# Kernel optimization log

Measured on AMD Instinct MI355X. Metric: run time of the kernel, lower is better.

Reference implementation:

```python
import jax, jax.numpy as jnp
import numpy as np

B, S, D, H, KD, FF = 512, 128, 128, 8, 128, 512  # molecules, max atoms, embed, heads, key_dim(=embed), ffn
NEG = -1e9
EPS = 1e-3  # keras LayerNormalization default epsilon


def _layernorm(x, g, b):
    m = jnp.mean(x, axis=-1, keepdims=True)
    v = jnp.var(x, axis=-1, keepdims=True)
    return (x - m) * jax.lax.rsqrt(v + EPS) * g + b


def setup_inputs() -> dict:
    key = jax.random.key(0)
    k = jax.random.split(key, 8)
    # ragged molecule sizes in [32, 128]; deterministic so shapes are reproducible
    counts = 32 + ((np.arange(B) * 37) % 97)
    N = int(counts.sum())  # 40914
    mol = jnp.asarray(np.repeat(np.arange(B), counts), jnp.int32)  # sorted molecule ids
    picked = jnp.asarray((np.arange(B) * 13) % counts, jnp.int64)  # valid in-molecule atom index
    s = 0.05
    return {
        "atom_features": jax.random.normal(k[0], (N, D), jnp.float32),
        "Wq": jax.random.normal(k[1], (D, H, KD), jnp.float32) * s,
        "bq": jnp.zeros((H, KD), jnp.float32),
        "Wk": jax.random.normal(k[2], (D, H, KD), jnp.float32) * s,
        "bk": jnp.zeros((H, KD), jnp.float32),
        "Wv": jax.random.normal(k[3], (D, H, KD), jnp.float32) * s,
        "bv": jnp.zeros((H, KD), jnp.float32),
        "Wo": jax.random.normal(k[4], (H, KD, D), jnp.float32) * s,
        "bo": jnp.zeros((D,), jnp.float32),
        "W1": jax.random.normal(k[5], (D, FF), jnp.float32) * s,
        "b1": jnp.zeros((FF,), jnp.float32),
        "W2": jax.random.normal(k[6], (FF, D), jnp.float32) * s,
        "b2": jnp.zeros((D,), jnp.float32),
        "g1": jnp.ones((D,), jnp.float32),
        "beta1": jnp.zeros((D,), jnp.float32),
        "g2": jnp.ones((D,), jnp.float32),
        "beta2": jnp.zeros((D,), jnp.float32),
        "molecule_indicator": mol,
        "picked_atoms": picked,
    }


def _forward(atom_features, Wq, bq, Wk, bk, Wv, bv, Wo, bo, W1, b1, W2, b2,
             g1, beta1, g2, beta2, mol, picked):
    N = mol.shape[0]
    # --- PartitionPadding: pack ragged atoms -> [B, S, D] (every molecule nonempty,
    # so the zero-row filter keeps all B molecules in order) ---
    counts = jax.ops.segment_sum(jnp.ones((N,), jnp.int32), mol, num_segments=B)
    offsets = jnp.concatenate([jnp.zeros((1,), jnp.int32), jnp.cumsum(counts)[:-1]])
    pos = jnp.arange(N, dtype=jnp.int32) - offsets[mol]  # index within molecule
    x = jnp.zeros((B, S, D), atom_features.dtype).at[mol, pos].set(atom_features)
    mask = jnp.arange(S)[None, :] < counts[:, None]  # key padding mask [B, S]

    # --- masked MHA (keras MultiHeadAttention, key_dim = embed_dim) ---
    q = jnp.einsum('bsd,dhk->bshk', x, Wq) + bq
    kk = jnp.einsum('bsd,dhk->bshk', x, Wk) + bk
    v = jnp.einsum('bsd,dhk->bshk', x, Wv) + bv
    scores = jnp.einsum('bqhk,bshk->bhqs', q, kk) / jnp.sqrt(jnp.float32(KD))
    scores = jnp.where(mask[:, None, None, :], scores, NEG)
    attn = jax.nn.softmax(scores, axis=-1)
    ctx = jnp.einsum('bhqs,bshk->bqhk', attn, v)
    attn_out = jnp.einsum('bqhk,hkd->bqd', ctx, Wo) + bo

    # --- residual + LN + FFN + LN ---
    h = _layernorm(x + attn_out, g1, beta1)
    ffn = jax.nn.relu(h @ W1 + b1) @ W2 + b2
    out = _layernorm(h + ffn, g2, beta2)

    # --- gather_nd readout: one picked atom per molecule ---
    return out[jnp.arange(B), picked]  # [B, D]


def reference(atom_features, Wq, bq, Wk, bk, Wv, bv, Wo, bo, W1, b1, W2, b2,
              g1, beta1, g2, beta2, molecule_indicator, picked_atoms):
    return _forward(atom_features, Wq, bq, Wk, bk, Wv, bv, Wo, bo, W1, b1, W2, b2,
                    g1, beta1, g2, beta2, molecule_indicator, picked_atoms)
```

## Files before the change

### kernel.cpp

```cpp
#include <hip/hip_runtime.h>
#include <hip/hip_bf16.h>
#include <hip/hip_fp16.h>


#define BMOL 512

typedef _Float16 v2h __attribute__((ext_vector_type(2)));
typedef _Float16 v8h __attribute__((ext_vector_type(8)));
typedef float f32x4 __attribute__((ext_vector_type(4)));

#if defined(__has_builtin)
#if __has_builtin(__builtin_amdgcn_fdot2)
#define HAVE_FDOT2 1
#endif
#endif
static __device__ __forceinline__ float fdot2f(v2h a, v2h b, float c) {
#ifdef HAVE_FDOT2
    return __builtin_amdgcn_fdot2(a, b, c, false);
#else
    return c + (float)a[0] * (float)b[0] + (float)a[1] * (float)b[1];
#endif
}

__global__ __launch_bounds__(256) void k_front(
    const float* __restrict__ Wq, const float* __restrict__ bq,
    const float* __restrict__ Wk, const float* __restrict__ Wv,
    const float* __restrict__ Wo, const float* __restrict__ bv,
    const float* __restrict__ W1, const float* __restrict__ W2,
    const int* __restrict__ mol, int N, int noff,
    int* __restrict__ offs, __half* __restrict__ WVOp,
    __half* __restrict__ WQKp, float* __restrict__ bqk,
    float* __restrict__ bvoP, __half* __restrict__ W1p, __half* __restrict__ W2p)
{
    __shared__ float lds[2176];
    int bid = blockIdx.x, t = threadIdx.x;

    if (bid < 256) {
        bool qk = bid >= 128;
        int rel = bid & 127;
        int h = rel >> 4, tile = rel & 15;
        int dt = tile >> 2, ct = tile & 3;
        float* Avs = lds;
        float* Bos = lds + 1056;
        int ry = t >> 5, cx = t & 31;
        float acc[4] = {0.f, 0.f, 0.f, 0.f};
        const float* Asrc = qk ? Wq : Wv;
        for (int kk = 0; kk < 4; ++kk) {
            int r = t >> 3, e0 = (t & 7) * 4;
            float4 va = *(const float4*)(Asrc + (size_t)(dt * 32 + r) * 1024 + h * 128 + kk * 32 + e0);
            Avs[r * 33 + e0] = va.x; Avs[r * 33 + e0 + 1] = va.y;
            Avs[r * 33 + e0 + 2] = va.z; Avs[r * 33 + e0 + 3] = va.w;
            if (qk) {
                float4 vb = *(const float4*)(Wk + (size_t)(ct * 32 + r) * 1024 + h * 128 + kk * 32 + e0);
                Bos[(e0 + 0) * 33 + r] = vb.x;
                Bos[(e0 + 1) * 33 + r] = vb.y;
                Bos[(e0 + 2) * 33 + r] = vb.z;
                Bos[(e0 + 3) * 33 + r] = vb.w;
            } else {
                float4 vb = *(const float4*)(Wo + (size_t)h * 16384 + (size_t)(kk * 32 + r) * 128 + ct * 32 + e0);
                Bos[r * 33 + e0] = vb.x; Bos[r * 33 + e0 + 1] = vb.y;
                Bos[r * 33 + e0 + 2] = vb.z; Bos[r * 33 + e0 + 3] = vb.w;
            }
            __syncthreads();
            #pragma unroll
            for (int k = 0; k < 32; ++k) {
                float b = Bos[k * 33 + cx];
                #pragma unroll
                for (int i = 0; i < 4; ++i) acc[i] += Avs[(ry * 4 + i) * 33 + k] * b;
            }
            __syncthreads();
        }
        __half2 p0 = __floats2half2_rn(acc[0], acc[1]);
        __half2 p1 = __floats2half2_rn(acc[2], acc[3]);
        __half* dst = (qk ? WQKp : WVOp)
                    + (size_t)(h * 16 + dt * 4 + (ry >> 1)) * 1024
                    + (ct * 32 + cx) * 8 + (ry & 1) * 4;
        ((__half2*)dst)[0] = p0; ((__half2*)dst)[1] = p1;
        return;
    }
    bid -= 256;
    if (bid < 32) {
        int g = bid * 256 + t;
        int kg = g >> 9, f = g & 511;
        __half2 p[4];
        #pragma unroll
        for (int j = 0; j < 4; ++j) {
            float a = W1[(size_t)(kg * 8 + 2 * j) * 512 + f];
            float b = W1[(size_t)(kg * 8 + 2 * j + 1) * 512 + f];
            p[j] = __floats2half2_rn(a, b);
        }
        *(float4*)(W1p + (size_t)kg * 4096 + f * 8) = *(float4*)p;
        return;
    }
    bid -= 32;
    if (bid < 32) {
        int g = bid * 256 + t;
        int fg = g >> 7, c = g & 127;
        __half2 p[4];
        #pragma unroll
        for (int j = 0; j < 4; ++j) {
            float a = W2[(size_t)(fg * 8 + 2 * j) * 128 + c];
            float b = W2[(size_t)(fg * 8 + 2 * j + 1) * 128 + c];
            p[j] = __floats2half2_rn(a, b);
        }
        *(float4*)(W2p + (size_t)fg * 1024 + c * 8) = *(float4*)p;
        return;
    }
    bid -= 32;
    if (bid < 8) {
        int half = t >> 7, c = t & 127;
        float acc = 0.f;
        #pragma unroll 4
        for (int kk = 0; kk < 64; ++kk) {
            int k = bid * 128 + half * 64 + kk;
            acc += bv[k] * Wo[(size_t)k * 128 + c];
        }
        lds[half * 128 + c] = acc;
        __syncthreads();
        if (t < 128) bvoP[bid * 128 + t] = lds[t] + lds[128 + t];
        return;
    }
    bid -= 8;
    if (bid < 8) {
        int h = bid;
        if (t < 128) {
            const float* wk = Wk + (size_t)t * 1024 + h * 128;
            const float* bqh = bq + h * 128;
            float acc = 0.f;
            #pragma unroll 4
            for (int kd = 0; kd < 128; ++kd) acc += bqh[kd] * wk[kd];
            bqk[h * 128 + t] = acc;
        }
        return;
    }
    bid -= 8;
    {
        int i = bid * 256 + t;
        if (i < N) {
            if (i == 0) { offs[0] = 0; offs[BMOL] = N; }
            else if (mol[i] != mol[i - 1]) offs[mol[i]] = i;
        }
    }
}

__global__ __launch_bounds__(512) void k_attn_tail(
    const float* __restrict__ AF, const int* __restrict__ offs,
    const int* __restrict__ picked,
    const __half* __restrict__ WQKp, const float* __restrict__ bqk,
    const __half* __restrict__ WVOp, const float* __restrict__ bvoP,
    const float* __restrict__ bo,
    const float* __restrict__ g1, const float* __restrict__ be1,
    const __half* __restrict__ W1p, const float* __restrict__ b1,
    const __half* __restrict__ W2p, const float* __restrict__ b2,
    const float* __restrict__ g2, const float* __restrict__ be2,
    float* __restrict__ out)
{
    int b = blockIdx.x, t = threadIdx.x;
    int o0 = offs[b], cnt = offs[b + 1] - o0;
    int cpad = ((cnt + 31) >> 5) << 5;
    __shared__ _Float16 xs[128][136];
    __shared__ _Float16 qsh[16][136];
    __shared__ float s[8 * 136];
    __shared__ _Float16 Ph[16][136];
    __shared__ float mh[8], lh[8];
    __shared__ _Float16 wsh[1024];
    __shared__ float part[4][128];
    __shared__ float xp[128];
    __shared__ _Float16 xph[128];
    __shared__ float h1raw[128], h1n[128];
    __shared__ _Float16 h1nh[128];
    __shared__ _Float16 msh[512];
    const float scale = 0.08838834764831843f;

    const float4* af4 = (const float4*)(AF + (size_t)o0 * 128);
    for (int p = t; p < cnt * 32; p += 512) {
        int i = p >> 5, d4 = p & 31;
        float4 v = af4[p];
        float2 st;
        ((__half2*)&st)[0] = __floats2half2_rn(v.x, v.y);
        ((__half2*)&st)[1] = __floats2half2_rn(v.z, v.w);
        *(float2*)(&xs[i][d4 * 4]) = st;
    }
    for (int p = cnt * 32 + t; p < cpad * 32; p += 512) {
        int i = p >> 5, d4 = p & 31;
        float2 z = {0.f, 0.f};
        *(float2*)(&xs[i][d4 * 4]) = z;
    }
    for (int p = t; p < 544; p += 512) {
        ((unsigned*)&qsh[8][0])[p] = 0u;
        ((unsigned*)&Ph[8][0])[p] = 0u;
    }
    if (t < 128) {
        float v = AF[(size_t)(o0 + picked[b]) * 128 + t];
        xp[t] = v; xph[t] = (_Float16)v;
    }
    __syncthreads();
    {
        int h = t >> 6, d0 = (t & 63) * 2;
        const __half* wp = WQKp + ((size_t)(h * 16) * 128 + d0) * 8;
        const v2h* xh = (const v2h*)xph;
        float a0 = 0.f, a1 = 0.f;
        #pragma unroll 4
        for (int kg = 0; kg < 16; ++kg) {
            float4 r0 = *(const float4*)(wp + (size_t)kg * 1024);
            float4 r1 = *(const float4*)(wp + (size_t)kg * 1024 + 8);
            const v2h* h0 = (const v2h*)&r0;
            const v2h* h1 = (const v2h*)&r1;
            #pragma unroll
            for (int j = 0; j < 4; ++j) {
                v2h xv = xh[kg * 4 + j];
                a0 = fdot2f(xv, h0[j], a0);
                a1 = fdot2f(xv, h1[j], a1);
            }
        }
        qsh[h][d0]     = (_Float16)((a0 + bqk[h * 128 + d0]) * scale);
        qsh[h][d0 + 1] = (_Float16)((a1 + bqk[h * 128 + d0 + 1]) * scale);
    }
    __syncthreads();
    {
        int w = t >> 6, l = t & 63;
        int i0 = w * 16;
        if (i0 < cnt) {
            int arow = i0 + (l & 15);
            int q = l >> 4;
            f32x4 acc = {0.f, 0.f, 0.f, 0.f};
            #pragma unroll
            for (int ks = 0; ks < 4; ++ks) {
                v8h a  = *(const v8h*)(&xs[arow][ks * 32 + q * 8]);
                v8h bf = *(const v8h*)(&qsh[l & 15][ks * 32 + q * 8]);
                acc = __builtin_amdgcn_mfma_f32_16x16x32_f16(a, bf, acc, 0, 0, 0);
            }
            if ((l & 15) < 8) {
                #pragma unroll
                for (int r = 0; r < 4; ++r)
                    s[(l & 15) * 136 + i0 + q * 4 + r] = acc[r];
            }
        }
    }
    __syncthreads();
    {
        int h = t >> 6, lane = t & 63;
        float m = -1e30f;
        for (int i = lane; i < cnt; i += 64) m = fmaxf(m, s[h * 136 + i]);
        #pragma unroll
        for (int off = 32; off; off >>= 1) m = fmaxf(m, __shfl_xor(m, off));
        float l = 0.f;
        for (int i = lane; i < cnt; i += 64) l += __expf(s[h * 136 + i] - m);
        #pragma unroll
        for (int off = 32; off; off >>= 1) l += __shfl_xor(l, off);
        if (lane == 0) { mh[h] = m; lh[h] = 1.f / l; }
    }
    __syncthreads();
    for (int p = t; p < cpad * 8; p += 512) {
        int i = p >> 3, h = p & 7;
        float v = (i < cnt) ? __expf(s[h * 136 + i] - mh[h]) * lh[h] : 0.f;
        Ph[h][i] = (_Float16)v;
    }
    __syncthreads();
    {
        int w = t >> 6, l = t & 63;
        int q = l >> 4;
        int d0 = w * 16 + (l & 15);
        int nks = cpad >> 5;
        f32x4 acc = {0.f, 0.f, 0.f, 0.f};
        for (int ks = 0; ks < nks; ++ks) {
            int k0 = ks * 32 + q * 8;
            v8h a = *(const v8h*)(&Ph[l & 15][k0]);
            v8h bf;
            #pragma unroll
            for (int j = 0; j < 8; ++j) bf[j] = xs[k0 + j][d0];
            acc = __builtin_amdgcn_mfma_f32_16x16x32_f16(a, bf, acc, 0, 0, 0);
        }
        #pragma unroll
        for (int r = 0; r < 4; ++r) {
            int h = q * 4 + r;
            if (h < 8) wsh[h * 128 + d0] = (_Float16)acc[r];
        }
    }
    __syncthreads();
    int wv = t >> 6, lane = t & 63;
    int kq = wv & 3, ch = wv >> 2;
    int c = ch * 64 + lane;
    {
        const __half* wp = WVOp + ((size_t)(kq * 32) * 128 + c) * 8;
        const v2h* wk = (const v2h*)wsh + kq * 128;
        float acc = 0.f;
        #pragma unroll 8
        for (int g = 0; g < 32; ++g) {
            float4 raw = *(const float4*)(wp + (size_t)g * 1024);
            const v2h* hp = (const v2h*)&raw;
            acc = fdot2f(hp[0], wk[g * 4 + 0], acc);
            acc = fdot2f(hp[1], wk[g * 4 + 1], acc);
            acc = fdot2f(hp[2], wk[g * 4 + 2], acc);
            acc = fdot2f(hp[3], wk[g * 4 + 3], acc);
        }
        part[kq][c] = acc;
    }
    __syncthreads();
    if (t < 128) {
        float acc = part[0][t] + part[1][t] + part[2][t] + part[3][t];
        float bias = bo[t];
        #pragma unroll
        for (int j = 0; j < 8; ++j) bias += bvoP[j * 128 + t];
        h1raw[t] = acc + bias + xp[t];
    }
    __syncthreads();
    {
        int l = t & 63;
        float a = h1raw[l], bb = h1raw[l + 64];
        float sm = a + bb, sq = a * a + bb * bb;
        #pragma unroll
        for (int off = 32; off; off >>= 1) { sm += __shfl_xor(sm, off); sq += __shfl_xor(sq, off); }
        float m = sm * (1.f / 128.f), var = sq * (1.f / 128.f) - m * m;
        float rs = rsqrtf(var + 1e-3f);
        if (t < 128) {
            float v = (h1raw[t] - m) * rs * g1[t] + be1[t];
            h1n[t] = v; h1nh[t] = (_Float16)v;
        }
    }
    __syncthreads();
    {
        const __half* wp = W1p + t * 8;
        const v2h* hk = (const v2h*)h1nh;
        float acc = 0.f;
        #pragma unroll 8
        for (int kg = 0; kg < 16; ++kg) {
            float4 raw = *(const float4*)(wp + (size_t)kg * 4096);
            const v2h* hp = (const v2h*)&raw;
            acc = fdot2f(hp[0], hk[kg * 4 + 0], acc);
            acc = fdot2f(hp[1], hk[kg * 4 + 1], acc);
            acc = fdot2f(hp[2], hk[kg * 4 + 2], acc);
            acc = fdot2f(hp[3], hk[kg * 4 + 3], acc);
        }
        msh[t] = (_Float16)fmaxf(acc + b1[t], 0.f);
    }
    __syncthreads();
    {
        const __half* wp = W2p + ((size_t)(kq * 16) * 128 + c) * 8;
        const v2h* mk = (const v2h*)msh + kq * 64;
        float acc = 0.f;
        #pragma unroll 8
        for (int g = 0; g < 16; ++g) {
            float4 raw = *(const float4*)(wp + (size_t)g * 1024);
            const v2h* hp = (const v2h*)&raw;
            acc = fdot2f(hp[0], mk[g * 4 + 0], acc);
            acc = fdot2f(hp[1], mk[g * 4 + 1], acc);
            acc = fdot2f(hp[2], mk[g * 4 + 2], acc);
            acc = fdot2f(hp[3], mk[g * 4 + 3], acc);
        }
        part[kq][c] = acc;
    }
    __syncthreads();
    if (t < 128) {
        float acc = part[0][t] + part[1][t] + part[2][t] + part[3][t];
        h1raw[t] = acc + b2[t] + h1n[t];
    }
    __syncthreads();
    {
        int l = t & 63;
        float a = h1raw[l], bb = h1raw[l + 64];
        float sm = a + bb, sq = a * a + bb * bb;
        #pragma unroll
        for (int off = 32; off; off >>= 1) { sm += __shfl_xor(sm, off); sq += __shfl_xor(sq, off); }
        float m = sm * (1.f / 128.f), var = sq * (1.f / 128.f) - m * m;
        float rs = rsqrtf(var + 1e-3f);
        if (t < 128) out[(size_t)b * 128 + t] = (h1raw[t] - m) * rs * g2[t] + be2[t];
    }
}

extern "C" void kernel_launch(void* const* d_in, const int* in_sizes, int n_in,
                              void* d_out, int out_size, void* d_ws, size_t ws_size,
                              hipStream_t stream) {
    const float* AF  = (const float*)d_in[0];
    const float* Wq  = (const float*)d_in[1];
    const float* bq  = (const float*)d_in[2];
    const float* Wk  = (const float*)d_in[3];
    const float* Wv  = (const float*)d_in[5];
    const float* bv  = (const float*)d_in[6];
    const float* Wo  = (const float*)d_in[7];
    const float* bo  = (const float*)d_in[8];
    const float* W1  = (const float*)d_in[9];
    const float* b1  = (const float*)d_in[10];
    const float* W2  = (const float*)d_in[11];
    const float* b2  = (const float*)d_in[12];
    const float* g1  = (const float*)d_in[13];
    const float* be1 = (const float*)d_in[14];
    const float* g2  = (const float*)d_in[15];
    const float* be2 = (const float*)d_in[16];
    const int* mol    = (const int*)d_in[17];
    const int* picked = (const int*)d_in[18];
    int N = in_sizes[0] / 128;
    int noff = (N + 255) / 256;

    char* ws = (char*)d_ws;
    int*    offs = (int*)ws;
    __half* WVOp = (__half*)(ws + 4096);
    __half* WQKp = (__half*)(ws + 266240);
    float*  bqk  = (float*)(ws + 528384);
    float*  bvoP = (float*)(ws + 532480);
    __half* W1p  = (__half*)(ws + 536576);
    __half* W2p  = (__half*)(ws + 667648);

    k_front<<<336 + noff, 256, 0, stream>>>(Wq, bq, Wk, Wv, Wo, bv, W1, W2,
                                            mol, N, noff,
                                            offs, WVOp, WQKp, bqk, bvoP, W1p, W2p);
    k_attn_tail<<<BMOL, 512, 0, stream>>>(AF, offs, picked, WQKp, bqk,
                                          WVOp, bvoP, bo, g1, be1, W1p, b1,
                                          W2p, b2, g2, be2, (float*)d_out);
}
```

Before: 32.52 us.

## Precompute per-molecule folded query vectors in front kernel with MFMA

The picked-atom query projection through the folded Wq·Wk^T matrix moves out of the attention kernel into 64 new front-kernel blocks. Each block finds molecule offsets by binary search, builds the folded QK matrix for one head in LDS with f16 MFMA, and multiplies it against 64 picked atoms, writing half-precision scaled queries to a workspace. The attention kernel then just loads the precomputed query rows, which removes one sync and a dot-product phase from its critical path. The cost is extra front-kernel work: the QK matrix is recomputed redundantly 8 times per head, and the front kernel now needs a large LDS allocation, which may lower occupancy of the other block types.

```diff
diff --git a/kernel.cpp b/kernel.cpp
--- a/kernel.cpp
+++ b/kernel.cpp
@@ -21,46 +21,44 @@
     return c + (float)a[0] * (float)b[0] + (float)a[1] * (float)b[1];
 #endif
 }
+static __device__ __forceinline__ v8h cvt8(const float* __restrict__ src) {
+    float4 f0 = *(const float4*)src, f1 = *(const float4*)(src + 4);
+    v8h a;
+    a[0] = (_Float16)f0.x; a[1] = (_Float16)f0.y; a[2] = (_Float16)f0.z; a[3] = (_Float16)f0.w;
+    a[4] = (_Float16)f1.x; a[5] = (_Float16)f1.y; a[6] = (_Float16)f1.z; a[7] = (_Float16)f1.w;
+    return a;
+}
 
 __global__ __launch_bounds__(256) void k_front(
-    const float* __restrict__ Wq, const float* __restrict__ bq,
-    const float* __restrict__ Wk, const float* __restrict__ Wv,
-    const float* __restrict__ Wo, const float* __restrict__ bv,
-    const float* __restrict__ W1, const float* __restrict__ W2,
-    const int* __restrict__ mol, int N, int noff,
+    const float* __restrict__ AF, const float* __restrict__ Wq,
+    const float* __restrict__ bq, const float* __restrict__ Wk,
+    const float* __restrict__ Wv, const float* __restrict__ Wo,
+    const float* __restrict__ bv, const float* __restrict__ W1,
+    const float* __restrict__ W2,
+    const int* __restrict__ mol, const int* __restrict__ picked,
+    int N, int noff,
     int* __restrict__ offs, __half* __restrict__ WVOp,
-    __half* __restrict__ WQKp, float* __restrict__ bqk,
-    float* __restrict__ bvoP, __half* __restrict__ W1p, __half* __restrict__ W2p)
+    float* __restrict__ bvoP, __half* __restrict__ W1p,
+    __half* __restrict__ W2p, __half* __restrict__ QKh)
 {
-    __shared__ float lds[2176];
+    __shared__ float smf[13312];
     int bid = blockIdx.x, t = threadIdx.x;
 
-    if (bid < 256) {
-        bool qk = bid >= 128;
-        int rel = bid & 127;
-        int h = rel >> 4, tile = rel & 15;
+    if (bid < 128) {
+        int h = bid >> 4, tile = bid & 15;
         int dt = tile >> 2, ct = tile & 3;
-        float* Avs = lds;
-        float* Bos = lds + 1056;
+        float* Avs = smf;
+        float* Bos = smf + 1056;
         int ry = t >> 5, cx = t & 31;
         float acc[4] = {0.f, 0.f, 0.f, 0.f};
-        const float* Asrc = qk ? Wq : Wv;
         for (int kk = 0; kk < 4; ++kk) {
             int r = t >> 3, e0 = (t & 7) * 4;
-            float4 va = *(const float4*)(Asrc + (size_t)(dt * 32 + r) * 1024 + h * 128 + kk * 32 + e0);
+            float4 va = *(const float4*)(Wv + (size_t)(dt * 32 + r) * 1024 + h * 128 + kk * 32 + e0);
             Avs[r * 33 + e0] = va.x; Avs[r * 33 + e0 + 1] = va.y;
             Avs[r * 33 + e0 + 2] = va.z; Avs[r * 33 + e0 + 3] = va.w;
-            if (qk) {
-                float4 vb = *(const float4*)(Wk + (size_t)(ct * 32 + r) * 1024 + h * 128 + kk * 32 + e0);
-                Bos[(e0 + 0) * 33 + r] = vb.x;
-                Bos[(e0 + 1) * 33 + r] = vb.y;
-                Bos[(e0 + 2) * 33 + r] = vb.z;
-                Bos[(e0 + 3) * 33 + r] = vb.w;
-            } else {
-                float4 vb = *(const float4*)(Wo + (size_t)h * 16384 + (size_t)(kk * 32 + r) * 128 + ct * 32 + e0);
-                Bos[r * 33 + e0] = vb.x; Bos[r * 33 + e0 + 1] = vb.y;
-                Bos[r * 33 + e0 + 2] = vb.z; Bos[r * 33 + e0 + 3] = vb.w;
-            }
+            float4 vb = *(const float4*)(Wo + (size_t)h * 16384 + (size_t)(kk * 32 + r) * 128 + ct * 32 + e0);
+            Bos[r * 33 + e0] = vb.x; Bos[r * 33 + e0 + 1] = vb.y;
+            Bos[r * 33 + e0 + 2] = vb.z; Bos[r * 33 + e0 + 3] = vb.w;
             __syncthreads();
             #pragma unroll
             for (int k = 0; k < 32; ++k) {
@@ -72,13 +70,94 @@
         }
         __half2 p0 = __floats2half2_rn(acc[0], acc[1]);
         __half2 p1 = __floats2half2_rn(acc[2], acc[3]);
-        __half* dst = (qk ? WQKp : WVOp)
-                    + (size_t)(h * 16 + dt * 4 + (ry >> 1)) * 1024
-                    + (ct * 32 + cx) * 8 + (ry & 1) * 4;
+        __half* dst = WVOp + (size_t)(h * 16 + dt * 4 + (ry >> 1)) * 1024
+                           + (ct * 32 + cx) * 8 + (ry & 1) * 4;
         ((__half2*)dst)[0] = p0; ((__half2*)dst)[1] = p1;
         return;
     }
-    bid -= 256;
+    bid -= 128;
+    if (bid < 64) {
+        int h = bid >> 3, mg = bid & 7;
+        int m0 = mg * 64;
+        _Float16* WQKT = (_Float16*)smf;
+        _Float16* xpl  = (_Float16*)((char*)smf + 34816);
+        float*    bqks = (float*)((char*)smf + 52224);
+        int*      rows = (int*)((char*)smf + 52736);
+        const float scale = 0.08838834764831843f;
+        if (t < 64) {
+            int m = m0 + t, lo = 0, hi = N;
+            while (lo < hi) { int mid = (lo + hi) >> 1; if (mol[mid] < m) lo = mid + 1; else hi = mid; }
+            rows[t] = lo + picked[m];
+        }
+        {
+            int d = t >> 1, half = t & 1;
+            const float* wk = Wk + (size_t)d * 1024 + h * 128 + half * 64;
+            const float* bqh = bq + h * 128 + half * 64;
+            float acc = 0.f;
+            #pragma unroll 4
+            for (int k = 0; k < 64; ++k) acc += bqh[k] * wk[k];
+            acc += __shfl_xor(acc, 1);
+            if (!half) bqks[d] = acc;
+        }
+        __syncthreads();
+        for (int p = t; p < 2048; p += 256) {
+            int m = p >> 5, d4 = p & 31;
+            float4 v = ((const float4*)(AF + (size_t)rows[m] * 128))[d4];
+            float2 st;
+            ((__half2*)&st)[0] = __floats2half2_rn(v.x, v.y);
+            ((__half2*)&st)[1] = __floats2half2_rn(v.z, v.w);
+            *(float2*)(&xpl[m * 136 + d4 * 4]) = st;
+        }
+        {
+            int w = t >> 6, l = t & 63, l15 = l & 15, q = l >> 4;
+            #pragma unroll
+            for (int dti = 0; dti < 2; ++dti) {
+                int dt = w * 2 + dti;
+                int drow = dt * 16 + l15;
+                v8h a0 = cvt8(Wk + (size_t)drow * 1024 + h * 128 + 0 * 32 + q * 8);
+                v8h a1 = cvt8(Wk + (size_t)drow * 1024 + h * 128 + 1 * 32 + q * 8);
+                v8h a2 = cvt8(Wk + (size_t)drow * 1024 + h * 128 + 2 * 32 + q * 8);
+                v8h a3 = cvt8(Wk + (size_t)drow * 1024 + h * 128 + 3 * 32 + q * 8);
+                for (int et = 0; et < 8; ++et) {
+                    int erow = et * 16 + l15;
+                    const float* wqr = Wq + (size_t)erow * 1024 + h * 128 + q * 8;
+                    f32x4 acc = {0.f, 0.f, 0.f, 0.f};
+                    acc = __builtin_amdgcn_mfma_f32_16x16x32_f16(a0, cvt8(wqr), acc, 0, 0, 0);
+                    acc = __builtin_amdgcn_mfma_f32_16x16x32_f16(a1, cvt8(wqr + 32), acc, 0, 0, 0);
+                    acc = __builtin_amdgcn_mfma_f32_16x16x32_f16(a2, cvt8(wqr + 64), acc, 0, 0, 0);
+                    acc = __builtin_amdgcn_mfma_f32_16x16x32_f16(a3, cvt8(wqr + 96), acc, 0, 0, 0);
+                    #pragma unroll
+                    for (int r = 0; r < 4; ++r)
+                        WQKT[(dt * 16 + q * 4 + r) * 136 + et * 16 + l15] = (_Float16)acc[r];
+                }
+            }
+        }
+        __syncthreads();
+        {
+            int w = t >> 6, l = t & 63, l15 = l & 15, q = l >> 4;
+            v8h a0 = *(const v8h*)(&xpl[(w * 16 + l15) * 136 + 0 * 32 + q * 8]);
+            v8h a1 = *(const v8h*)(&xpl[(w * 16 + l15) * 136 + 1 * 32 + q * 8]);
+            v8h a2 = *(const v8h*)(&xpl[(w * 16 + l15) * 136 + 2 * 32 + q * 8]);
+            v8h a3 = *(const v8h*)(&xpl[(w * 16 + l15) * 136 + 3 * 32 + q * 8]);
+            for (int dt2 = 0; dt2 < 8; ++dt2) {
+                const _Float16* wrow = &WQKT[(dt2 * 16 + l15) * 136 + q * 8];
+                f32x4 acc = {0.f, 0.f, 0.f, 0.f};
+                acc = __builtin_amdgcn_mfma_f32_16x16x32_f16(a0, *(const v8h*)(wrow), acc, 0, 0, 0);
+                acc = __builtin_amdgcn_mfma_f32_16x16x32_f16(a1, *(const v8h*)(wrow + 32), acc, 0, 0, 0);
+                acc = __builtin_amdgcn_mfma_f32_16x16x32_f16(a2, *(const v8h*)(wrow + 64), acc, 0, 0, 0);
+                acc = __builtin_amdgcn_mfma_f32_16x16x32_f16(a3, *(const v8h*)(wrow + 96), acc, 0, 0, 0);
+                int d = dt2 * 16 + l15;
+                #pragma unroll
+                for (int r = 0; r < 4; ++r) {
+                    int m = w * 16 + q * 4 + r;
+                    QKh[(size_t)(m0 + m) * 1024 + h * 128 + d] =
+                        (__half)((acc[r] + bqks[d]) * scale);
+                }
+            }
+        }
+        return;
+    }
+    bid -= 64;
     if (bid < 32) {
         int g = bid * 256 + t;
         int kg = g >> 9, f = g & 511;
@@ -115,22 +194,9 @@
             int k = bid * 128 + half * 64 + kk;
             acc += bv[k] * Wo[(size_t)k * 128 + c];
         }
-        lds[half * 128 + c] = acc;
+        smf[half * 128 + c] = acc;
         __syncthreads();
-        if (t < 128) bvoP[bid * 128 + t] = lds[t] + lds[128 + t];
-        return;
-    }
-    bid -= 8;
-    if (bid < 8) {
-        int h = bid;
-        if (t < 128) {
-            const float* wk = Wk + (size_t)t * 1024 + h * 128;
-            const float* bqh = bq + h * 128;
-            float acc = 0.f;
-            #pragma unroll 4
-            for (int kd = 0; kd < 128; ++kd) acc += bqh[kd] * wk[kd];
-            bqk[h * 128 + t] = acc;
-        }
+        if (t < 128) bvoP[bid * 128 + t] = smf[t] + smf[128 + t];
         return;
     }
     bid -= 8;
@@ -145,8 +211,7 @@
 
 __global__ __launch_bounds__(512) void k_attn_tail(
     const float* __restrict__ AF, const int* __restrict__ offs,
-    const int* __restrict__ picked,
-    const __half* __restrict__ WQKp, const float* __restrict__ bqk,
+    const int* __restrict__ picked, const __half* __restrict__ QKh,
     const __half* __restrict__ WVOp, const float* __restrict__ bvoP,
     const float* __restrict__ bo,
     const float* __restrict__ g1, const float* __restrict__ be1,
@@ -166,11 +231,9 @@
     __shared__ _Float16 wsh[1024];
     __shared__ float part[4][128];
     __shared__ float xp[128];
-    __shared__ _Float16 xph[128];
     __shared__ float h1raw[128], h1n[128];
     __shared__ _Float16 h1nh[128];
     __shared__ _Float16 msh[512];
-    const float scale = 0.08838834764831843f;
 
     const float4* af4 = (const float4*)(AF + (size_t)o0 * 128);
     for (int p = t; p < cnt * 32; p += 512) {
@@ -191,31 +254,11 @@
         ((unsigned*)&Ph[8][0])[p] = 0u;
     }
     if (t < 128) {
-        float v = AF[(size_t)(o0 + picked[b]) * 128 + t];
-        xp[t] = v; xph[t] = (_Float16)v;
-    }
-    __syncthreads();
-    {
-        int h = t >> 6, d0 = (t & 63) * 2;
-        const __half* wp = WQKp + ((size_t)(h * 16) * 128 + d0) * 8;
-        const v2h* xh = (const v2h*)xph;
-        float a0 = 0.f, a1 = 0.f;
-        #pragma unroll 4
-        for (int kg = 0; kg < 16; ++kg) {
-            float4 r0 = *(const float4*)(wp + (size_t)kg * 1024);
-            float4 r1 = *(const float4*)(wp + (size_t)kg * 1024 + 8);
-            const v2h* h0 = (const v2h*)&r0;
-            const v2h* h1 = (const v2h*)&r1;
-            #pragma unroll
-            for (int j = 0; j < 4; ++j) {
-                v2h xv = xh[kg * 4 + j];
-                a0 = fdot2f(xv, h0[j], a0);
-                a1 = fdot2f(xv, h1[j], a1);
-            }
-        }
-        qsh[h][d0]     = (_Float16)((a0 + bqk[h * 128 + d0]) * scale);
-        qsh[h][d0 + 1] = (_Float16)((a1 + bqk[h * 128 + d0 + 1]) * scale);
-    }
+        float4 ld = ((const float4*)(QKh + (size_t)b * 1024))[t];
+        int hh = t >> 4, d0 = (t & 15) * 8;
+        *(float4*)(&qsh[hh][d0]) = ld;
+    }
+    if (t < 128) xp[t] = AF[(size_t)(o0 + picked[b]) * 128 + t];
     __syncthreads();
     {
         int w = t >> 6, l = t & 63;
@@ -395,16 +438,15 @@
     char* ws = (char*)d_ws;
     int*    offs = (int*)ws;
     __half* WVOp = (__half*)(ws + 4096);
-    __half* WQKp = (__half*)(ws + 266240);
-    float*  bqk  = (float*)(ws + 528384);
-    float*  bvoP = (float*)(ws + 532480);
-    __half* W1p  = (__half*)(ws + 536576);
-    __half* W2p  = (__half*)(ws + 667648);
-
-    k_front<<<336 + noff, 256, 0, stream>>>(Wq, bq, Wk, Wv, Wo, bv, W1, W2,
-                                            mol, N, noff,
-                                            offs, WVOp, WQKp, bqk, bvoP, W1p, W2p);
-    k_attn_tail<<<BMOL, 512, 0, stream>>>(AF, offs, picked, WQKp, bqk,
+    float*  bvoP = (float*)(ws + 266240);
+    __half* W1p  = (__half*)(ws + 270336);
+    __half* W2p  = (__half*)(ws + 401408);
+    __half* QKh  = (__half*)(ws + 532480);
+
+    k_front<<<264 + noff, 256, 0, stream>>>(AF, Wq, bq, Wk, Wv, Wo, bv, W1, W2,
+                                            mol, picked, N, noff,
+                                            offs, WVOp, bvoP, W1p, W2p, QKh);
+    k_attn_tail<<<BMOL, 512, 0, stream>>>(AF, offs, picked, QKh,
                                           WVOp, bvoP, bo, g1, be1, W1p, b1,
                                           W2p, b2, g2, be2, (float*)d_out);
 }
```

After: 57.06 us. 1.75x slower.
